# Kernel optimization log

Hardware: AMD Instinct MI355X
Metric: run time of the kernel (lower is better)

The kernel has to match this reference:

```python
import jax, jax.numpy as jnp
import numpy as np

N = 4096
NUM_FEATURES = 1870
HIDDEN = 256
EMBED = 16
ALPHA = 0.2
NEG_BIG = -9e15
EPS = 1e-12


def setup_inputs() -> dict:
    key = jax.random.key(0)
    ks = jax.random.split(key, 9)
    x = jax.random.normal(ks[0], (N, NUM_FEATURES), dtype=jnp.float32)
    # sparse-ish binary adjacency mask (avg degree ~ 41) with self loops
    adj = (jax.random.uniform(ks[1], (N, N)) < 0.01).astype(jnp.float32)
    adj = jnp.maximum(adj, jnp.eye(N, dtype=jnp.float32))
    M = jax.random.uniform(ks[2], (N, N), dtype=jnp.float32)
    s1 = 1.0 / np.sqrt(NUM_FEATURES)
    s2 = 1.0 / np.sqrt(HIDDEN)
    W1 = jax.random.normal(ks[3], (NUM_FEATURES, HIDDEN), dtype=jnp.float32) * s1
    a_self1 = jax.random.normal(ks[4], (HIDDEN, 1), dtype=jnp.float32) * s2
    a_neighs1 = jax.random.normal(ks[5], (HIDDEN, 1), dtype=jnp.float32) * s2
    W2 = jax.random.normal(ks[6], (HIDDEN, EMBED), dtype=jnp.float32) * s2
    a_self2 = jax.random.normal(ks[7], (EMBED, 1), dtype=jnp.float32) / np.sqrt(EMBED)
    a_neighs2 = jax.random.normal(ks[8], (EMBED, 1), dtype=jnp.float32) / np.sqrt(EMBED)
    return {"x": x, "adj": adj, "M": M, "W1": W1, "a_self1": a_self1,
            "a_neighs1": a_neighs1, "W2": W2, "a_self2": a_self2, "a_neighs2": a_neighs2}


def gat_layer(x, adj, M, W, a_self, a_neighs, alpha):
    h = x @ W                                  # [N, out]
    f_self = h @ a_self                        # [N, 1]
    f_neigh = h @ a_neighs                     # [N, 1]
    e = jax.nn.leaky_relu((f_self + f_neigh.T) * M, negative_slope=alpha)  # [N, N]
    e = jnp.where(adj > 0, e, NEG_BIG)
    att = jax.nn.softmax(e, axis=1)            # row-stochastic over neighbors
    return jax.nn.elu(att @ h)                 # [N, out]


def reference(x, adj, M, W1, a_self1, a_neighs1, W2, a_self2, a_neighs2):
    h = gat_layer(x, adj, M, W1, a_self1, a_neighs1, ALPHA)
    h = gat_layer(h, adj, M, W2, a_self2, a_neighs2, ALPHA)
    # F.normalize(h, p=2, dim=1): divide by max(norm, eps)
    norm = jnp.maximum(jnp.linalg.norm(h, axis=1, keepdims=True), EPS)
    z = h / norm                               # [N, EMBED]
    A_pred = jax.nn.sigmoid(z @ z.T)           # [N, N]
    return (A_pred, z)
```

## Files before the change

### kernel.cpp

```cpp
#include <hip/hip_runtime.h>
#include <math.h>

#define NN 4096
#define NFEAT 1870
#define KB2 2048
#define KSPLIT 8
#define KCHUNK 256
#define BK 32
#define HID 256
#define EMB 16
#define MAXDEG 128

typedef __attribute__((ext_vector_type(8))) _Float16 f16x8;
typedef __attribute__((ext_vector_type(4))) float f32x4;

__device__ __forceinline__ ushort f2h(float f) {
    _Float16 h = (_Float16)f;
    return __builtin_bit_cast(ushort, h);
}

__device__ __forceinline__ void gload_lds16(const void* g, void* l) {
    __builtin_amdgcn_global_load_lds(
        (const __attribute__((address_space(1))) unsigned int*)g,
        (__attribute__((address_space(3))) unsigned int*)l, 16, 0, 0);
}

__global__ __launch_bounds__(256) void extract_kernel(
    const float* __restrict__ adj, const float* __restrict__ Mmat,
    int* __restrict__ nnz, int* __restrict__ gidx, float* __restrict__ Mg)
{
    const int tid = threadIdx.x;
    const int wv = tid >> 6, lane = tid & 63;
    const int row = blockIdx.x * 4 + wv;
    const float* arow = adj + (size_t)row * NN + lane * 64;

    unsigned long long mask = 0;
#pragma unroll
    for (int i = 0; i < 16; ++i) {
        float4 v = *(const float4*)&arow[i * 4];
        if (v.x > 0.f) mask |= 1ull << (i * 4 + 0);
        if (v.y > 0.f) mask |= 1ull << (i * 4 + 1);
        if (v.z > 0.f) mask |= 1ull << (i * 4 + 2);
        if (v.w > 0.f) mask |= 1ull << (i * 4 + 3);
    }
    const int cnt = __popcll(mask);
    int incl = cnt;
#pragma unroll
    for (int off = 1; off < 64; off <<= 1) {
        int y = __shfl_up(incl, off, 64);
        if (lane >= off) incl += y;
    }
    if (lane == 63) nnz[row] = min(incl, MAXDEG);
    int base = incl - cnt;

    const float* mrow = Mmat + (size_t)row * NN + lane * 64;
    unsigned long long mm = mask;
    int off = base;
    while (mm) {
        int bit = __ffsll((unsigned long long)mm) - 1;
        mm &= mm - 1;
        if (off < MAXDEG) {
            gidx[(size_t)row * MAXDEG + off] = lane * 64 + bit;
            Mg[(size_t)row * MAXDEG + off] = mrow[bit];
        }
        ++off;
    }
}

__global__ __launch_bounds__(256) void xcv_kernel(
    const float* __restrict__ x, ushort* __restrict__ xf)
{
    const int row = blockIdx.x;
    const int tid = threadIdx.x;
    const int c0 = tid * 8;
    float v[8];
    if (c0 + 8 <= NFEAT) {
#pragma unroll
        for (int j = 0; j < 4; ++j) {
            float2 t = *(const float2*)&x[(size_t)row * NFEAT + c0 + j * 2];
            v[j * 2] = t.x; v[j * 2 + 1] = t.y;
        }
    } else {
#pragma unroll
        for (int j = 0; j < 8; ++j)
            v[j] = (c0 + j < NFEAT) ? x[(size_t)row * NFEAT + c0 + j] : 0.f;
    }
    ushort u[8];
#pragma unroll
    for (int j = 0; j < 8; ++j) u[j] = f2h(v[j]);
    *(int4*)&xf[(size_t)row * KB2 + c0] = *(int4*)u;
}

__global__ __launch_bounds__(256) void w1t_kernel(
    const float* __restrict__ W1, ushort* __restrict__ Wh)
{
    __shared__ float t[64][65];
    const int bb = blockIdx.x;
    const int tid = threadIdx.x;
    const int k0 = (bb & 31) * 64, n0 = (bb >> 5) * 64;
    const int kk = tid >> 2, c4 = (tid & 3) * 16;
#pragma unroll
    for (int j = 0; j < 4; ++j) {
        int k = k0 + kk;
        float4 v = make_float4(0.f, 0.f, 0.f, 0.f);
        if (k < NFEAT) v = *(const float4*)&W1[(size_t)k * HID + n0 + c4 + j * 4];
        t[kk][c4 + j * 4 + 0] = v.x; t[kk][c4 + j * 4 + 1] = v.y;
        t[kk][c4 + j * 4 + 2] = v.z; t[kk][c4 + j * 4 + 3] = v.w;
    }
    __syncthreads();
    const int on = tid >> 2, ok4 = (tid & 3) * 16;
#pragma unroll
    for (int j = 0; j < 4; ++j) {
        ushort hh[4];
#pragma unroll
        for (int i = 0; i < 4; ++i)
            hh[i] = f2h(t[ok4 + j * 4 + i][on]);
        size_t o = (size_t)(n0 + on) * KB2 + k0 + ok4 + j * 4;
        *(ushort4*)&Wh[o] = *(ushort4*)hh;
    }
}

__global__ __launch_bounds__(256, 2) void gemm_xw1(
    const ushort* __restrict__ Ag,
    const ushort* __restrict__ Bg,
    float* __restrict__ Cpart)
{
    __shared__ ushort Ah[128 * BK];
    __shared__ ushort Bh[128 * BK];
    const int tid = threadIdx.x;
    const int lane = tid & 63;
    const int w = tid >> 6;
    const int wr = w >> 1, wc = w & 1;
    const int row0 = blockIdx.x * 128;
    const int col0 = blockIdx.y * 128;
    const int kbeg = blockIdx.z * KCHUNK;
    const int fr = lane & 15, fs = lane >> 4;

    f32x4 acc[4][4] = {};

    for (int ks = 0; ks < KCHUNK / BK; ++ks) {
        const int k0 = kbeg + ks * BK;
        __syncthreads();
#pragma unroll
        for (int i = 0; i < 2; ++i) {
            int idx = i * 256 + tid;
            int r = idx >> 2, t = idx & 3;
            int kslot = (t ^ (r & 3)) * 8;
            gload_lds16(&Ag[(size_t)(row0 + r) * KB2 + k0 + kslot], &Ah[idx * 8]);
            gload_lds16(&Bg[(size_t)(col0 + r) * KB2 + k0 + kslot], &Bh[idx * 8]);
        }
        __syncthreads();
        f16x8 af[4], bf[4];
#pragma unroll
        for (int m = 0; m < 4; ++m) {
            int r = wr * 64 + m * 16 + fr;
            af[m] = *(const f16x8*)&Ah[r * BK + ((fs ^ (r & 3)) * 8)];
        }
#pragma unroll
        for (int n = 0; n < 4; ++n) {
            int r = wc * 64 + n * 16 + fr;
            bf[n] = *(const f16x8*)&Bh[r * BK + ((fs ^ (r & 3)) * 8)];
        }
#pragma unroll
        for (int m = 0; m < 4; ++m)
#pragma unroll
            for (int n = 0; n < 4; ++n)
                acc[m][n] = __builtin_amdgcn_mfma_f32_16x16x32_f16(
                    af[m], bf[n], acc[m][n], 0, 0, 0);
    }
    float* Cp = Cpart + (size_t)blockIdx.z * NN * HID;
#pragma unroll
    for (int m = 0; m < 4; ++m)
#pragma unroll
        for (int n = 0; n < 4; ++n)
#pragma unroll
            for (int r = 0; r < 4; ++r) {
                int row = row0 + wr * 64 + m * 16 + fs * 4 + r;
                int col = col0 + wc * 64 + n * 16 + fr;
                Cp[(size_t)row * HID + col] = acc[m][n][r];
            }
}

__global__ __launch_bounds__(256) void reduce_h1f_kernel(
    const float* __restrict__ part, float* __restrict__ h1,
    const float* __restrict__ a_s, const float* __restrict__ a_n,
    float* __restrict__ fs, float* __restrict__ fn)
{
    const int tid = threadIdx.x, wv = tid >> 6, lane = tid & 63;
    const int row = blockIdx.x * 4 + wv;
    const int d0 = lane * 4;
    const size_t o = (size_t)row * HID + d0;
    float4 s = *(const float4*)&part[o];
#pragma unroll
    for (int ch = 1; ch < KSPLIT; ++ch) {
        float4 p = *(const float4*)&part[(size_t)ch * NN * HID + o];
        s.x += p.x; s.y += p.y; s.z += p.z; s.w += p.w;
    }
    *(float4*)&h1[o] = s;
    float4 as4 = *(const float4*)&a_s[d0];
    float4 an4 = *(const float4*)&a_n[d0];
    float ps = s.x * as4.x + s.y * as4.y + s.z * as4.z + s.w * as4.w;
    float pn = s.x * an4.x + s.y * an4.y + s.z * an4.z + s.w * an4.w;
#pragma unroll
    for (int off = 32; off > 0; off >>= 1) {
        ps += __shfl_down(ps, off, 64);
        pn += __shfl_down(pn, off, 64);
    }
    if (lane == 0) { fs[row] = ps; fn[row] = pn; }
}

__global__ __launch_bounds__(256) void spmm1_kernel(
    const int* __restrict__ nnz, const int* __restrict__ gidx,
    const float* __restrict__ Mg,
    const float* __restrict__ fs, const float* __restrict__ fn,
    const float* __restrict__ h1, float* __restrict__ g1)
{
    __shared__ float p_s[MAXDEG];
    __shared__ int j_s[MAXDEG];
    __shared__ float wred[4], wsum[4];
    const int row = blockIdx.x;
    const int tid = threadIdx.x;
    const int lane = tid & 63, wv = tid >> 6;
    const int cnt = nnz[row];
    const float fsi = fs[row];

    float lmax = -3.0e38f;
    for (int s = tid; s < cnt; s += 256) {
        int j = gidx[(size_t)row * MAXDEG + s];
        j_s[s] = j;
        float e = (fsi + fn[j]) * Mg[(size_t)row * MAXDEG + s];
        e = (e > 0.f) ? e : 0.2f * e;
        p_s[s] = e;
        lmax = fmaxf(lmax, e);
    }
#pragma unroll
    for (int off = 32; off > 0; off >>= 1)
        lmax = fmaxf(lmax, __shfl_down(lmax, off, 64));
    if (lane == 0) wred[wv] = lmax;
    __syncthreads();
    const float m = fmaxf(fmaxf(wred[0], wred[1]), fmaxf(wred[2], wred[3]));

    float lsum = 0.f;
    for (int s = tid; s < cnt; s += 256) {
        float p = __expf(p_s[s] - m);
        p_s[s] = p;
        lsum += p;
    }
#pragma unroll
    for (int off = 32; off > 0; off >>= 1)
        lsum += __shfl_down(lsum, off, 64);
    if (lane == 0) wsum[wv] = lsum;
    __syncthreads();
    const float inv = 1.f / (wsum[0] + wsum[1] + wsum[2] + wsum[3]);

    float acc = 0.f;
#pragma unroll 4
    for (int s = 0; s < cnt; ++s)
        acc += p_s[s] * h1[(size_t)j_s[s] * HID + tid];
    float v = acc * inv;
    v = (v > 0.f) ? v : (__expf(v) - 1.f);
    g1[(size_t)row * HID + tid] = v;
}

__global__ __launch_bounds__(256) void gemm_h2_kernel(
    const float* __restrict__ g1, const float* __restrict__ W2,
    const float* __restrict__ a_s2, const float* __restrict__ a_n2,
    float* __restrict__ h2, float* __restrict__ fs2, float* __restrict__ fn2)
{
    __shared__ float Ws[256][16];
    __shared__ float Gs[16][257];
    const int tid = threadIdx.x;
    const int row0 = blockIdx.x * 16;
#pragma unroll
    for (int i = 0; i < 16; ++i) {
        int idx = tid + i * 256;
        Ws[idx >> 4][idx & 15] = W2[idx];
    }
#pragma unroll
    for (int i = 0; i < 16; ++i) {
        int idx = tid + i * 256;
        Gs[idx >> 8][idx & 255] = g1[(size_t)(row0 + (idx >> 8)) * HID + (idx & 255)];
    }
    __syncthreads();
    const int r = tid >> 4, c = tid & 15;
    float acc = 0.f;
#pragma unroll 8
    for (int k = 0; k < 256; ++k)
        acc += Gs[r][k] * Ws[k][c];
    h2[(size_t)(row0 + r) * EMB + c] = acc;

    float ps = acc * a_s2[c];
    float pn = acc * a_n2[c];
#pragma unroll
    for (int off = 1; off < 16; off <<= 1) {
        ps += __shfl_xor(ps, off, 64);
        pn += __shfl_xor(pn, off, 64);
    }
    if (c == 0) { fs2[row0 + r] = ps; fn2[row0 + r] = pn; }
}

__global__ __launch_bounds__(256) void spmm2_kernel(
    const int* __restrict__ nnz, const int* __restrict__ gidx,
    const float* __restrict__ Mg,
    const float* __restrict__ fs, const float* __restrict__ fn,
    const float* __restrict__ h2, float* __restrict__ z)
{
    __shared__ float p_s[4][MAXDEG];
    __shared__ int j_s[4][MAXDEG];
    const int tid = threadIdx.x;
    const int wv = tid >> 6, lane = tid & 63;
    const int row = blockIdx.x * 4 + wv;
    const int cnt = nnz[row];
    const float fsi = fs[row];

    float lmax = -3.0e38f;
    for (int s = lane; s < cnt; s += 64) {
        int j = gidx[(size_t)row * MAXDEG + s];
        j_s[wv][s] = j;
        float e = (fsi + fn[j]) * Mg[(size_t)row * MAXDEG + s];
        e = (e > 0.f) ? e : 0.2f * e;
        p_s[wv][s] = e;
        lmax = fmaxf(lmax, e);
    }
#pragma unroll
    for (int off = 1; off < 64; off <<= 1)
        lmax = fmaxf(lmax, __shfl_xor(lmax, off, 64));

    float lsum = 0.f;
    for (int s = lane; s < cnt; s += 64) {
        float p = __expf(p_s[wv][s] - lmax);
        p_s[wv][s] = p;
        lsum += p;
    }
#pragma unroll
    for (int off = 1; off < 64; off <<= 1)
        lsum += __shfl_xor(lsum, off, 64);
    const float inv = 1.f / lsum;

    const int s0 = lane >> 4, d = lane & 15;
    float acc = 0.f;
    for (int s = s0; s < cnt; s += 4)
        acc += p_s[wv][s] * h2[(size_t)j_s[wv][s] * EMB + d];
    acc += __shfl_xor(acc, 16, 64);
    acc += __shfl_xor(acc, 32, 64);

    float v = acc * inv;
    v = (v > 0.f) ? v : (__expf(v) - 1.f);
    float ss = v * v;
#pragma unroll
    for (int off = 1; off < 16; off <<= 1)
        ss += __shfl_xor(ss, off, 64);
    float zn = v / fmaxf(sqrtf(ss), 1e-12f);
    if (lane < 16) z[(size_t)row * EMB + lane] = zn;
}

__global__ __launch_bounds__(256) void apred_kernel(
    const float* __restrict__ z, float* __restrict__ out)
{
    __shared__ float zr[64][20];
    __shared__ float zc[64][20];
    const int tid = threadIdx.x;
    const int r0 = blockIdx.y * 64, c0 = blockIdx.x * 64;
#pragma unroll
    for (int i = 0; i < 4; ++i) {
        int idx = tid + i * 256;
        int rr = idx >> 4, d = idx & 15;
        zr[rr][d] = z[(size_t)(r0 + rr) * EMB + d];
        zc[rr][d] = z[(size_t)(c0 + rr) * EMB + d];
    }
    __syncthreads();
    const int tx = tid & 15, ty = tid >> 4;
    float rb[4][16], cb[4][16];
#pragma unroll
    for (int i = 0; i < 4; ++i)
#pragma unroll
        for (int d = 0; d < 16; ++d) {
            rb[i][d] = zr[ty * 4 + i][d];
            cb[i][d] = zc[tx * 4 + i][d];
        }
#pragma unroll
    for (int i = 0; i < 4; ++i) {
        float4 o;
        float v[4];
#pragma unroll
        for (int j = 0; j < 4; ++j) {
            float s = 0.f;
#pragma unroll
            for (int d = 0; d < 16; ++d) s += rb[i][d] * cb[j][d];
            v[j] = 1.f / (1.f + __expf(-s));
        }
        o.x = v[0]; o.y = v[1]; o.z = v[2]; o.w = v[3];
        *reinterpret_cast<float4*>(
            &out[(size_t)(r0 + ty * 4 + i) * NN + c0 + tx * 4]) = o;
    }
}

extern "C" void kernel_launch(void* const* d_in, const int* in_sizes, int n_in,
                              void* d_out, int out_size, void* d_ws, size_t ws_size,
                              hipStream_t stream)
{
    const float* x    = (const float*)d_in[0];
    const float* adj  = (const float*)d_in[1];
    const float* Mm   = (const float*)d_in[2];
    const float* W1   = (const float*)d_in[3];
    const float* a_s1 = (const float*)d_in[4];
    const float* a_n1 = (const float*)d_in[5];
    const float* W2   = (const float*)d_in[6];
    const float* a_s2 = (const float*)d_in[7];
    const float* a_n2 = (const float*)d_in[8];

    float* out = (float*)d_out;
    float* z   = out + (size_t)NN * NN;
    float* part = out;

    char* w = (char*)d_ws;
    float* h1    = (float*)w;  w += (size_t)NN * HID * 4;
    float* g1    = (float*)w;  w += (size_t)NN * HID * 4;
    ushort* xf16 = (ushort*)w; w += (size_t)NN * KB2 * 2;
    ushort* W1Th = (ushort*)w; w += (size_t)HID * KB2 * 2;
    float* h2    = (float*)w;  w += (size_t)NN * EMB * 4;
    int*   nnzp  = (int*)w;    w += NN * 4;
    int*   gidx  = (int*)w;    w += (size_t)NN * MAXDEG * 4;
    float* Mg    = (float*)w;  w += (size_t)NN * MAXDEG * 4;
    float* fs1   = (float*)w;  w += NN * 4;
    float* fn1   = (float*)w;  w += NN * 4;
    float* fs2   = (float*)w;  w += NN * 4;
    float* fn2   = (float*)w;  w += NN * 4;

    xcv_kernel<<<NN, 256, 0, stream>>>(x, xf16);
    w1t_kernel<<<128, 256, 0, stream>>>(W1, W1Th);
    extract_kernel<<<NN / 4, 256, 0, stream>>>(adj, Mm, nnzp, gidx, Mg);

    gemm_xw1<<<dim3(32, 2, KSPLIT), 256, 0, stream>>>(xf16, W1Th, part);
    reduce_h1f_kernel<<<NN / 4, 256, 0, stream>>>(part, h1, a_s1, a_n1, fs1, fn1);
    spmm1_kernel<<<NN, 256, 0, stream>>>(nnzp, gidx, Mg, fs1, fn1, h1, g1);

    gemm_h2_kernel<<<256, 256, 0, stream>>>(g1, W2, a_s2, a_n2, h2, fs2, fn2);
    spmm2_kernel<<<NN / 4, 256, 0, stream>>>(nnzp, gidx, Mg, fs2, fn2, h2, z);

    apred_kernel<<<dim3(64, 64), 256, 0, stream>>>(z, out);
}
```

Measured before the change: 104.0 us.

## Fuse prep kernels and build coalesced adjacency bitmasks, deferring compaction to spmm1

The x-conversion, W1-transpose and adjacency-extraction kernels become one launch, partitioned by block index. Adjacency rows are now read with coalesced float4 loads, and each lane's predicates are packed into 64-bit ballot masks. Compacting the masks into neighbour indices, and gathering the M values, now happens inside spmm1, which also writes gidx/Mg for reuse by spmm2. This removes two launches, the strided per-lane adjacency reads and a separate M gather pass. The cost is extra serial bit-scan work on one wave at the start of each spmm1 block and a changed neighbour summation order.

```diff
diff --git a/kernel.cpp b/kernel.cpp
--- a/kernel.cpp
+++ b/kernel.cpp
@@ -25,98 +25,73 @@
         (__attribute__((address_space(3))) unsigned int*)l, 16, 0, 0);
 }
 
-__global__ __launch_bounds__(256) void extract_kernel(
-    const float* __restrict__ adj, const float* __restrict__ Mmat,
-    int* __restrict__ nnz, int* __restrict__ gidx, float* __restrict__ Mg)
-{
-    const int tid = threadIdx.x;
-    const int wv = tid >> 6, lane = tid & 63;
-    const int row = blockIdx.x * 4 + wv;
-    const float* arow = adj + (size_t)row * NN + lane * 64;
-
-    unsigned long long mask = 0;
-#pragma unroll
-    for (int i = 0; i < 16; ++i) {
-        float4 v = *(const float4*)&arow[i * 4];
-        if (v.x > 0.f) mask |= 1ull << (i * 4 + 0);
-        if (v.y > 0.f) mask |= 1ull << (i * 4 + 1);
-        if (v.z > 0.f) mask |= 1ull << (i * 4 + 2);
-        if (v.w > 0.f) mask |= 1ull << (i * 4 + 3);
-    }
-    const int cnt = __popcll(mask);
-    int incl = cnt;
-#pragma unroll
-    for (int off = 1; off < 64; off <<= 1) {
-        int y = __shfl_up(incl, off, 64);
-        if (lane >= off) incl += y;
-    }
-    if (lane == 63) nnz[row] = min(incl, MAXDEG);
-    int base = incl - cnt;
-
-    const float* mrow = Mmat + (size_t)row * NN + lane * 64;
-    unsigned long long mm = mask;
-    int off = base;
-    while (mm) {
-        int bit = __ffsll((unsigned long long)mm) - 1;
-        mm &= mm - 1;
-        if (off < MAXDEG) {
-            gidx[(size_t)row * MAXDEG + off] = lane * 64 + bit;
-            Mg[(size_t)row * MAXDEG + off] = mrow[bit];
-        }
-        ++off;
-    }
-}
-
-__global__ __launch_bounds__(256) void xcv_kernel(
-    const float* __restrict__ x, ushort* __restrict__ xf)
-{
-    const int row = blockIdx.x;
-    const int tid = threadIdx.x;
-    const int c0 = tid * 8;
-    float v[8];
-    if (c0 + 8 <= NFEAT) {
+__global__ __launch_bounds__(256) void prep_kernel(
+    const float* __restrict__ adj, unsigned long long* __restrict__ masks,
+    const float* __restrict__ x, ushort* __restrict__ xf,
+    const float* __restrict__ W1, ushort* __restrict__ Wh)
+{
+    const int b = blockIdx.x;
+    const int tid = threadIdx.x;
+    if (b < NN / 4) {
+        const int wv = tid >> 6, lane = tid & 63;
+        const int row = b * 4 + wv;
+        const float* arow = adj + (size_t)row * NN;
+        unsigned long long* mrow = masks + (size_t)row * 64;
+#pragma unroll
+        for (int i = 0; i < 16; ++i) {
+            float4 v = *(const float4*)&arow[(size_t)(i * 64 + lane) * 4];
+            unsigned long long b0 = __ballot(v.x > 0.f);
+            unsigned long long b1 = __ballot(v.y > 0.f);
+            unsigned long long b2 = __ballot(v.z > 0.f);
+            unsigned long long b3 = __ballot(v.w > 0.f);
+            if (lane == 0) {
+                mrow[i * 4 + 0] = b0; mrow[i * 4 + 1] = b1;
+                mrow[i * 4 + 2] = b2; mrow[i * 4 + 3] = b3;
+            }
+        }
+    } else if (b < NN / 4 + NN) {
+        const int row = b - NN / 4;
+        const int c0 = tid * 8;
+        float v[8];
+        if (c0 + 8 <= NFEAT) {
+#pragma unroll
+            for (int j = 0; j < 4; ++j) {
+                float2 t = *(const float2*)&x[(size_t)row * NFEAT + c0 + j * 2];
+                v[j * 2] = t.x; v[j * 2 + 1] = t.y;
+            }
+        } else {
+#pragma unroll
+            for (int j = 0; j < 8; ++j)
+                v[j] = (c0 + j < NFEAT) ? x[(size_t)row * NFEAT + c0 + j] : 0.f;
+        }
+        ushort u[8];
+#pragma unroll
+        for (int j = 0; j < 8; ++j) u[j] = f2h(v[j]);
+        *(int4*)&xf[(size_t)row * KB2 + c0] = *(int4*)u;
+    } else {
+        __shared__ float t[64][65];
+        const int bb = b - NN / 4 - NN;
+        const int k0 = (bb & 31) * 64, n0 = (bb >> 5) * 64;
+        const int kk = tid >> 2, c4 = (tid & 3) * 16;
 #pragma unroll
         for (int j = 0; j < 4; ++j) {
-            float2 t = *(const float2*)&x[(size_t)row * NFEAT + c0 + j * 2];
-            v[j * 2] = t.x; v[j * 2 + 1] = t.y;
-        }
-    } else {
-#pragma unroll
-        for (int j = 0; j < 8; ++j)
-            v[j] = (c0 + j < NFEAT) ? x[(size_t)row * NFEAT + c0 + j] : 0.f;
-    }
-    ushort u[8];
-#pragma unroll
-    for (int j = 0; j < 8; ++j) u[j] = f2h(v[j]);
-    *(int4*)&xf[(size_t)row * KB2 + c0] = *(int4*)u;
-}
-
-__global__ __launch_bounds__(256) void w1t_kernel(
-    const float* __restrict__ W1, ushort* __restrict__ Wh)
-{
-    __shared__ float t[64][65];
-    const int bb = blockIdx.x;
-    const int tid = threadIdx.x;
-    const int k0 = (bb & 31) * 64, n0 = (bb >> 5) * 64;
-    const int kk = tid >> 2, c4 = (tid & 3) * 16;
-#pragma unroll
-    for (int j = 0; j < 4; ++j) {
-        int k = k0 + kk;
-        float4 v = make_float4(0.f, 0.f, 0.f, 0.f);
-        if (k < NFEAT) v = *(const float4*)&W1[(size_t)k * HID + n0 + c4 + j * 4];
-        t[kk][c4 + j * 4 + 0] = v.x; t[kk][c4 + j * 4 + 1] = v.y;
-        t[kk][c4 + j * 4 + 2] = v.z; t[kk][c4 + j * 4 + 3] = v.w;
-    }
-    __syncthreads();
-    const int on = tid >> 2, ok4 = (tid & 3) * 16;
-#pragma unroll
-    for (int j = 0; j < 4; ++j) {
-        ushort hh[4];
-#pragma unroll
-        for (int i = 0; i < 4; ++i)
-            hh[i] = f2h(t[ok4 + j * 4 + i][on]);
-        size_t o = (size_t)(n0 + on) * KB2 + k0 + ok4 + j * 4;
-        *(ushort4*)&Wh[o] = *(ushort4*)hh;
+            int k = k0 + kk;
+            float4 v = make_float4(0.f, 0.f, 0.f, 0.f);
+            if (k < NFEAT) v = *(const float4*)&W1[(size_t)k * HID + n0 + c4 + j * 4];
+            t[kk][c4 + j * 4 + 0] = v.x; t[kk][c4 + j * 4 + 1] = v.y;
+            t[kk][c4 + j * 4 + 2] = v.z; t[kk][c4 + j * 4 + 3] = v.w;
+        }
+        __syncthreads();
+        const int on = tid >> 2, ok4 = (tid & 3) * 16;
+#pragma unroll
+        for (int j = 0; j < 4; ++j) {
+            ushort hh[4];
+#pragma unroll
+            for (int i = 0; i < 4; ++i)
+                hh[i] = f2h(t[ok4 + j * 4 + i][on]);
+            size_t o = (size_t)(n0 + on) * KB2 + k0 + ok4 + j * 4;
+            *(ushort4*)&Wh[o] = *(ushort4*)hh;
+        }
     }
 }
 
@@ -210,25 +185,55 @@
 }
 
 __global__ __launch_bounds__(256) void spmm1_kernel(
-    const int* __restrict__ nnz, const int* __restrict__ gidx,
-    const float* __restrict__ Mg,
+    const unsigned long long* __restrict__ masks,
+    const float* __restrict__ Mmat,
     const float* __restrict__ fs, const float* __restrict__ fn,
-    const float* __restrict__ h1, float* __restrict__ g1)
+    const float* __restrict__ h1,
+    int* __restrict__ nnz, int* __restrict__ gidx, float* __restrict__ MgG,
+    float* __restrict__ g1)
 {
     __shared__ float p_s[MAXDEG];
     __shared__ int j_s[MAXDEG];
     __shared__ float wred[4], wsum[4];
+    __shared__ int cnt_s;
     const int row = blockIdx.x;
     const int tid = threadIdx.x;
     const int lane = tid & 63, wv = tid >> 6;
-    const int cnt = nnz[row];
+
+    if (wv == 0) {
+        unsigned long long m = masks[(size_t)row * 64 + lane];
+        const int c = __popcll(m);
+        int incl = c;
+#pragma unroll
+        for (int off = 1; off < 64; off <<= 1) {
+            int y = __shfl_up(incl, off, 64);
+            if (lane >= off) incl += y;
+        }
+        int off = incl - c;
+        const int i = lane >> 2, cc = lane & 3;
+        while (m) {
+            int l = __ffsll(m) - 1;
+            m &= m - 1;
+            if (off < MAXDEG) j_s[off] = (i * 64 + l) * 4 + cc;
+            ++off;
+        }
+        if (lane == 63) {
+            int t = min(incl, MAXDEG);
+            cnt_s = t;
+            nnz[row] = t;
+        }
+    }
+    __syncthreads();
+    const int cnt = cnt_s;
     const float fsi = fs[row];
 
     float lmax = -3.0e38f;
     for (int s = tid; s < cnt; s += 256) {
-        int j = gidx[(size_t)row * MAXDEG + s];
-        j_s[s] = j;
-        float e = (fsi + fn[j]) * Mg[(size_t)row * MAXDEG + s];
+        int j = j_s[s];
+        float mv = Mmat[(size_t)row * NN + j];
+        gidx[(size_t)row * MAXDEG + s] = j;
+        MgG[(size_t)row * MAXDEG + s] = mv;
+        float e = (fsi + fn[j]) * mv;
         e = (e > 0.f) ? e : 0.2f * e;
         p_s[s] = e;
         lmax = fmaxf(lmax, e);
@@ -419,6 +424,8 @@
     ushort* xf16 = (ushort*)w; w += (size_t)NN * KB2 * 2;
     ushort* W1Th = (ushort*)w; w += (size_t)HID * KB2 * 2;
     float* h2    = (float*)w;  w += (size_t)NN * EMB * 4;
+    unsigned long long* masks = (unsigned long long*)w;
+    w += (size_t)NN * 64 * 8;
     int*   nnzp  = (int*)w;    w += NN * 4;
     int*   gidx  = (int*)w;    w += (size_t)NN * MAXDEG * 4;
     float* Mg    = (float*)w;  w += (size_t)NN * MAXDEG * 4;
@@ -427,13 +434,13 @@
     float* fs2   = (float*)w;  w += NN * 4;
     float* fn2   = (float*)w;  w += NN * 4;
 
-    xcv_kernel<<<NN, 256, 0, stream>>>(x, xf16);
-    w1t_kernel<<<128, 256, 0, stream>>>(W1, W1Th);
-    extract_kernel<<<NN / 4, 256, 0, stream>>>(adj, Mm, nnzp, gidx, Mg);
+    prep_kernel<<<NN / 4 + NN + 128, 256, 0, stream>>>(
+        adj, masks, x, xf16, W1, W1Th);
 
     gemm_xw1<<<dim3(32, 2, KSPLIT), 256, 0, stream>>>(xf16, W1Th, part);
     reduce_h1f_kernel<<<NN / 4, 256, 0, stream>>>(part, h1, a_s1, a_n1, fs1, fn1);
-    spmm1_kernel<<<NN, 256, 0, stream>>>(nnzp, gidx, Mg, fs1, fn1, h1, g1);
+    spmm1_kernel<<<NN, 256, 0, stream>>>(masks, Mm, fs1, fn1, h1,
+                                         nnzp, gidx, Mg, g1);
 
     gemm_h2_kernel<<<256, 256, 0, stream>>>(g1, W2, a_s2, a_n2, h2, fs2, fn2);
     spmm2_kernel<<<NN / 4, 256, 0, stream>>>(nnzp, gidx, Mg, fs2, fn2, h2, z);
```

After: 96.56 us. -7.1%, faster.
